# Performance work log

Hardware: AMD Instinct MI355X
Metric: run time of the kernel (lower is better)

## Reference

```python
import jax, jax.numpy as jnp
import numpy as np

N_C, N_S, D = 16384, 16384, 2688  # 128x128 hypercolumn grid, VGG16 concat channels
EPS = 1e-8


def setup_inputs() -> dict:
    key = jax.random.key(0)
    k1, k2 = jax.random.split(key)
    feats_c = jax.random.normal(k1, (N_C, D), dtype=jnp.float32)
    feats_s = jax.random.normal(k2, (N_S, D), dtype=jnp.float32)
    return {"feats_c": feats_c, "feats_s": feats_s}


def reference(feats_c, feats_s):
    # NNST replace_features: for each content hypercolumn vector, find the
    # style feature vector with max cosine similarity and take it as target.
    cn = feats_c * jax.lax.rsqrt(jnp.sum(feats_c * feats_c, axis=1, keepdims=True) + EPS)
    sn = feats_s * jax.lax.rsqrt(jnp.sum(feats_s * feats_s, axis=1, keepdims=True) + EPS)
    sim = jnp.einsum("cd,sd->cs", cn, sn)  # [N_C, N_S] cosine similarity
    idx = jnp.argmax(sim, axis=1)           # nearest style feature per content pixel
    target_feats = jnp.take(feats_s, idx, axis=0)  # gather un-normalized style feats
    return target_feats
```

## Files before the change

kernel.cpp:

```cpp
#include <hip/hip_runtime.h>
#include <stdint.h>

typedef unsigned short ushort_t;
typedef unsigned int u32;
typedef unsigned long long u64;

#define NC_ 16384
#define NS_ 16384
#define DIM 2688
#define D4 (DIM / 4)
#define KSTEPS (DIM / 32)

typedef __attribute__((ext_vector_type(8))) short short8;
typedef __attribute__((ext_vector_type(4))) float f32x4;


__device__ inline ushort_t f2bf(float x) {
  u32 u = __float_as_uint(x);
  u32 r = u + 0x7FFFu + ((u >> 16) & 1u);
  return (ushort_t)(r >> 16);
}
__device__ inline float bf2f(ushort_t b) { return __uint_as_float(((u32)b) << 16); }

__device__ inline u32 fkey(float f) {
  u32 u = __float_as_uint(f);
  return (u & 0x80000000u) ? ~u : (u | 0x80000000u);
}

__device__ inline void async16(const void* g, void* l) {
  __builtin_amdgcn_global_load_lds(
      (const __attribute__((address_space(1))) u32*)g,
      (__attribute__((address_space(3))) u32*)l, 16, 0, 0);
}

__device__ inline int swz(int r, int q) {
  return ((r >> 1) << 6) + (((((r & 1) << 2) | q) ^ ((r >> 1) & 7)) << 3);
}


__global__ __launch_bounds__(256) void content_split_kernel(
    const float* __restrict__ fc, ushort_t* __restrict__ c_hi, ushort_t* __restrict__ c_lo) {
  size_t i = (size_t)blockIdx.x * 256 + threadIdx.x;
  if (i >= (size_t)NC_ * DIM / 4) return;
  float4 v = ((const float4*)fc)[i];
  ushort4 h, l;
  h.x = f2bf(v.x); l.x = f2bf(v.x - bf2f(h.x));
  h.y = f2bf(v.y); l.y = f2bf(v.y - bf2f(h.y));
  h.z = f2bf(v.z); l.z = f2bf(v.z - bf2f(h.z));
  h.w = f2bf(v.w); l.w = f2bf(v.w - bf2f(h.w));
  ((ushort4*)c_hi)[i] = h;
  ((ushort4*)c_lo)[i] = l;
}


__global__ __launch_bounds__(256) void style_split_kernel(
    const float* __restrict__ fs, ushort_t* __restrict__ s_hi, ushort_t* __restrict__ s_lo) {
  const int s = blockIdx.x, t = threadIdx.x;
  const float4* row = (const float4*)(fs + (size_t)s * DIM);
  float ss = 0.f;
  for (int i = t; i < D4; i += 256) {
    float4 v = row[i];
    ss += v.x * v.x + v.y * v.y + v.z * v.z + v.w * v.w;
  }
#pragma unroll
  for (int off = 32; off >= 1; off >>= 1) ss += __shfl_xor(ss, off, 64);
  __shared__ float wsum[4];
  if ((t & 63) == 0) wsum[t >> 6] = ss;
  __syncthreads();
  float scale = rsqrtf(wsum[0] + wsum[1] + wsum[2] + wsum[3] + 1e-8f);
  ushort4* h4 = (ushort4*)(s_hi + (size_t)s * DIM);
  ushort4* l4 = (ushort4*)(s_lo + (size_t)s * DIM);
  for (int i = t; i < D4; i += 256) {
    float4 v = row[i];
    float x = v.x * scale, y = v.y * scale, z = v.z * scale, w = v.w * scale;
    ushort4 h, l;
    h.x = f2bf(x); l.x = f2bf(x - bf2f(h.x));
    h.y = f2bf(y); l.y = f2bf(y - bf2f(h.y));
    h.z = f2bf(z); l.z = f2bf(z - bf2f(h.z));
    h.w = f2bf(w); l.w = f2bf(w - bf2f(h.w));
    h4[i] = h;
    l4[i] = l;
  }
}


__global__ __launch_bounds__(256, 2) void sim_argmax_kernel(
    const ushort_t* __restrict__ c_hi, const ushort_t* __restrict__ c_lo,
    const ushort_t* __restrict__ s_hi, const ushort_t* __restrict__ s_lo,
    u64* __restrict__ partial) {
  __shared__ __align__(16) ushort_t lds[24576];

  ushort_t* la_hi = lds;
  ushort_t* la_lo = lds + 4096;
  ushort_t* lb_hi = lds + 8192;
  ushort_t* lb_lo = lds + 16384;
  u64 (*red)[2] = (u64(*)[2])lds;

  const int t = threadIdx.x;
  const int bid = blockIdx.x;
  const int grp = bid >> 8;
  const int wi = bid & 255;
  const int cb = (grp & 7) * 16 + (wi & 15);
  const int sb = (grp >> 3) * 16 + (wi >> 4);

  const ushort_t* gah = c_hi + (size_t)cb * 128 * DIM;
  const ushort_t* gal = c_lo + (size_t)cb * 128 * DIM;
  const ushort_t* gbh = s_hi + (size_t)sb * 256 * DIM;
  const ushort_t* gbl = s_lo + (size_t)sb * 256 * DIM;

  const int lane = t & 63;
  const int wave = t >> 6;
  const int wy = wave >> 1, wx = wave & 1;
  const int lm = lane & 15, q = lane >> 4;

  f32x4 acc[4][8];
#pragma unroll
  for (int i = 0; i < 4; i++)
#pragma unroll
    for (int j = 0; j < 8; j++) acc[i][j] = (f32x4){0.f, 0.f, 0.f, 0.f};

  const int tw = t & 192;

  for (int ks = 0; ks < KSTEPS; ++ks) {
    const int kel = ks * 32;
#pragma unroll
    for (int j = 0; j < 2; ++j) {
      int e = j * 256 + t;
      int rp = e >> 3;
      int cc = (e & 7) ^ (rp & 7);
      int row = (rp << 1) | (cc >> 2);
      size_t goff = (size_t)row * DIM + kel + (cc & 3) * 8;
      int loff = (j * 256 + tw) * 8;
      async16(gah + goff, la_hi + loff);
      async16(gal + goff, la_lo + loff);
    }
#pragma unroll
    for (int j = 0; j < 4; ++j) {
      int e = j * 256 + t;
      int rp = e >> 3;
      int cc = (e & 7) ^ (rp & 7);
      int row = (rp << 1) | (cc >> 2);
      size_t goff = (size_t)row * DIM + kel + (cc & 3) * 8;
      int loff = (j * 256 + tw) * 8;
      async16(gbh + goff, lb_hi + loff);
      async16(gbl + goff, lb_lo + loff);
    }
    __syncthreads();

    short8 ah[4], al[4];
#pragma unroll
    for (int mi = 0; mi < 4; ++mi) {
      int r = swz(wy * 64 + mi * 16 + lm, q);
      ah[mi] = *(const short8*)(la_hi + r);
      al[mi] = *(const short8*)(la_lo + r);
    }
#pragma unroll
    for (int h = 0; h < 2; ++h) {
      short8 bh[4], bl[4];
#pragma unroll
      for (int nj = 0; nj < 4; ++nj) {
        int r = swz(wx * 128 + (h * 4 + nj) * 16 + lm, q);
        bh[nj] = *(const short8*)(lb_hi + r);
        bl[nj] = *(const short8*)(lb_lo + r);
      }
#pragma unroll
      for (int mi = 0; mi < 4; ++mi)
#pragma unroll
        for (int nj = 0; nj < 4; ++nj) {
          int ni = h * 4 + nj;
          acc[mi][ni] = __builtin_amdgcn_mfma_f32_16x16x32_bf16(ah[mi], bh[nj], acc[mi][ni], 0, 0, 0);
          acc[mi][ni] = __builtin_amdgcn_mfma_f32_16x16x32_bf16(ah[mi], bl[nj], acc[mi][ni], 0, 0, 0);
          acc[mi][ni] = __builtin_amdgcn_mfma_f32_16x16x32_bf16(al[mi], bh[nj], acc[mi][ni], 0, 0, 0);
        }
    }
    __syncthreads();
  }

#pragma unroll
  for (int mi = 0; mi < 4; ++mi) {
#pragma unroll
    for (int r = 0; r < 4; ++r) {
      float bv = acc[mi][0][r];
      int bn = 0;
#pragma unroll
      for (int ni = 1; ni < 8; ++ni) {
        float v = acc[mi][ni][r];
        if (v > bv) { bv = v; bn = ni; }
      }
      u32 colg = (u32)(sb * 256 + wx * 128 + bn * 16 + lm);
      u64 key = ((u64)fkey(bv) << 32) | (u64)(0xFFFFFFFFu - colg);
#pragma unroll
      for (int off = 8; off >= 1; off >>= 1) {
        u64 o = __shfl_xor((unsigned long long)key, off, 64);
        if (o > key) key = o;
      }
      if (lm == 0) red[wy * 64 + mi * 16 + q * 4 + r][wx] = key;
    }
  }
  __syncthreads();
  if (t < 128) {
    u64 k0 = red[t][0], k1 = red[t][1];
    u64 b = k0 > k1 ? k0 : k1;
    partial[((size_t)(cb * 128 + t)) * 64 + sb] = b;
  }
}


__global__ __launch_bounds__(256) void argmax_gather_kernel(
    const u64* __restrict__ partial, const float* __restrict__ fs, float* __restrict__ out) {
  const int m = blockIdx.x, t = threadIdx.x;
  __shared__ u64 sbest;
  if (t < 64) {
    u64 key = partial[(size_t)m * 64 + t];
#pragma unroll
    for (int off = 32; off >= 1; off >>= 1) {
      u64 o = __shfl_xor((unsigned long long)key, off, 64);
      if (o > key) key = o;
    }
    if (t == 0) sbest = key;
  }
  __syncthreads();
  u64 best = sbest;
  u32 col = 0xFFFFFFFFu - (u32)best;
  const float4* src = (const float4*)(fs + (size_t)col * DIM);
  float4* dst = (float4*)(out + (size_t)m * DIM);
  for (int i = t; i < D4; i += 256) dst[i] = src[i];
}


extern "C" void kernel_launch(void* const* d_in, const int* in_sizes, int n_in,
                              void* d_out, int out_size, void* d_ws, size_t ws_size,
                              hipStream_t stream) {
  const float* fc = (const float*)d_in[0];
  const float* fs = (const float*)d_in[1];
  float* out = (float*)d_out;

  ushort_t* c_hi = (ushort_t*)d_ws;
  ushort_t* c_lo = c_hi + (size_t)NC_ * DIM;
  ushort_t* s_hi = c_lo + (size_t)NC_ * DIM;
  ushort_t* s_lo = s_hi + (size_t)NS_ * DIM;
  u64* partial = (u64*)(s_lo + (size_t)NS_ * DIM);

  content_split_kernel<<<(NC_ * DIM / 4 + 255) / 256, 256, 0, stream>>>(fc, c_hi, c_lo);
  style_split_kernel<<<NS_, 256, 0, stream>>>(fs, s_hi, s_lo);
  sim_argmax_kernel<<<8192, 256, 0, stream>>>(c_hi, c_lo, s_hi, s_lo, partial);
  argmax_gather_kernel<<<NC_, 256, 0, stream>>>(partial, fs, out);
}
```

Before: 3.799 ms.

## Enlarge similarity tile to 256x256 with double-buffered async LDS prefetch

The similarity/argmax kernel now uses 512-thread blocks computing 256x256 content-by-style tiles, instead of 256-thread blocks on 128x256 tiles. This raises data reuse per loaded K-slice. The LDS is split into two buffers so the global-to-LDS async loads for step k+1 are issued before computing step k. A vmcnt wait plus barriers replace the per-step syncthreads. The larger LDS footprint (about 136KB) likely allows only one block per CU, so occupancy drops, and the cross-wave reduction grows to four columns.

```diff
diff --git a/kernel.cpp b/kernel.cpp
--- a/kernel.cpp
+++ b/kernel.cpp
@@ -84,124 +84,122 @@
 }
 
 
-__global__ __launch_bounds__(256, 2) void sim_argmax_kernel(
+__global__ __launch_bounds__(512, 2) void sim_argmax_kernel(
     const ushort_t* __restrict__ c_hi, const ushort_t* __restrict__ c_lo,
     const ushort_t* __restrict__ s_hi, const ushort_t* __restrict__ s_lo,
     u64* __restrict__ partial) {
-  __shared__ __align__(16) ushort_t lds[24576];
-
-  ushort_t* la_hi = lds;
-  ushort_t* la_lo = lds + 4096;
-  ushort_t* lb_hi = lds + 8192;
-  ushort_t* lb_lo = lds + 16384;
-  u64 (*red)[2] = (u64(*)[2])lds;
+  __shared__ __align__(16) ushort_t lds[65536];
+  __shared__ u64 red[256][4];
 
   const int t = threadIdx.x;
   const int bid = blockIdx.x;
-  const int grp = bid >> 8;
-  const int wi = bid & 255;
-  const int cb = (grp & 7) * 16 + (wi & 15);
-  const int sb = (grp >> 3) * 16 + (wi >> 4);
-
-  const ushort_t* gah = c_hi + (size_t)cb * 128 * DIM;
-  const ushort_t* gal = c_lo + (size_t)cb * 128 * DIM;
+  const int grp = bid >> 6;
+  const int wi = bid & 63;
+  const int cb = (grp & 7) * 8 + (wi & 7);
+  const int sb = (grp >> 3) * 8 + (wi >> 3);
+
+  const ushort_t* gah = c_hi + (size_t)cb * 256 * DIM;
+  const ushort_t* gal = c_lo + (size_t)cb * 256 * DIM;
   const ushort_t* gbh = s_hi + (size_t)sb * 256 * DIM;
   const ushort_t* gbl = s_lo + (size_t)sb * 256 * DIM;
 
   const int lane = t & 63;
   const int wave = t >> 6;
-  const int wy = wave >> 1, wx = wave & 1;
+  const int wy = wave >> 2, wx = wave & 3;
   const int lm = lane & 15, q = lane >> 4;
-
-  f32x4 acc[4][8];
-#pragma unroll
-  for (int i = 0; i < 4; i++)
-#pragma unroll
-    for (int j = 0; j < 8; j++) acc[i][j] = (f32x4){0.f, 0.f, 0.f, 0.f};
-
-  const int tw = t & 192;
-
-  for (int ks = 0; ks < KSTEPS; ++ks) {
+  const int wb = t & 448;
+
+  f32x4 acc[8][4];
+#pragma unroll
+  for (int i = 0; i < 8; i++)
+#pragma unroll
+    for (int j = 0; j < 4; j++) acc[i][j] = (f32x4){0.f, 0.f, 0.f, 0.f};
+
+  auto stage = [&](int ks, int b) {
     const int kel = ks * 32;
+    ushort_t* base = lds + b * 32768;
 #pragma unroll
     for (int j = 0; j < 2; ++j) {
-      int e = j * 256 + t;
+      int e = j * 512 + t;
       int rp = e >> 3;
       int cc = (e & 7) ^ (rp & 7);
       int row = (rp << 1) | (cc >> 2);
       size_t goff = (size_t)row * DIM + kel + (cc & 3) * 8;
-      int loff = (j * 256 + tw) * 8;
-      async16(gah + goff, la_hi + loff);
-      async16(gal + goff, la_lo + loff);
-    }
-#pragma unroll
-    for (int j = 0; j < 4; ++j) {
-      int e = j * 256 + t;
-      int rp = e >> 3;
-      int cc = (e & 7) ^ (rp & 7);
-      int row = (rp << 1) | (cc >> 2);
-      size_t goff = (size_t)row * DIM + kel + (cc & 3) * 8;
-      int loff = (j * 256 + tw) * 8;
-      async16(gbh + goff, lb_hi + loff);
-      async16(gbl + goff, lb_lo + loff);
-    }
-    __syncthreads();
-
-    short8 ah[4], al[4];
-#pragma unroll
-    for (int mi = 0; mi < 4; ++mi) {
-      int r = swz(wy * 64 + mi * 16 + lm, q);
-      ah[mi] = *(const short8*)(la_hi + r);
-      al[mi] = *(const short8*)(la_lo + r);
-    }
-#pragma unroll
-    for (int h = 0; h < 2; ++h) {
-      short8 bh[4], bl[4];
-#pragma unroll
-      for (int nj = 0; nj < 4; ++nj) {
-        int r = swz(wx * 128 + (h * 4 + nj) * 16 + lm, q);
-        bh[nj] = *(const short8*)(lb_hi + r);
-        bl[nj] = *(const short8*)(lb_lo + r);
+      int loff = (j * 512 + wb) * 8;
+      async16(gah + goff, base + loff);
+      async16(gal + goff, base + 8192 + loff);
+      async16(gbh + goff, base + 16384 + loff);
+      async16(gbl + goff, base + 24576 + loff);
+    }
+  };
+
+  auto compute = [&](int b) {
+    ushort_t* base = lds + b * 32768;
+    const ushort_t* lah = base;
+    const ushort_t* lal = base + 8192;
+    const ushort_t* lbh = base + 16384;
+    const ushort_t* lbl = base + 24576;
+    short8 ah[8], al[8];
+#pragma unroll
+    for (int mi = 0; mi < 8; ++mi) {
+      int r = swz(wy * 128 + mi * 16 + lm, q);
+      ah[mi] = *(const short8*)(lah + r);
+      al[mi] = *(const short8*)(lal + r);
+    }
+#pragma unroll
+    for (int nj = 0; nj < 4; ++nj) {
+      int r = swz(wx * 64 + nj * 16 + lm, q);
+      short8 bh = *(const short8*)(lbh + r);
+      short8 bl = *(const short8*)(lbl + r);
+#pragma unroll
+      for (int mi = 0; mi < 8; ++mi) {
+        acc[mi][nj] = __builtin_amdgcn_mfma_f32_16x16x32_bf16(ah[mi], bh, acc[mi][nj], 0, 0, 0);
+        acc[mi][nj] = __builtin_amdgcn_mfma_f32_16x16x32_bf16(ah[mi], bl, acc[mi][nj], 0, 0, 0);
+        acc[mi][nj] = __builtin_amdgcn_mfma_f32_16x16x32_bf16(al[mi], bh, acc[mi][nj], 0, 0, 0);
       }
-#pragma unroll
-      for (int mi = 0; mi < 4; ++mi)
-#pragma unroll
-        for (int nj = 0; nj < 4; ++nj) {
-          int ni = h * 4 + nj;
-          acc[mi][ni] = __builtin_amdgcn_mfma_f32_16x16x32_bf16(ah[mi], bh[nj], acc[mi][ni], 0, 0, 0);
-          acc[mi][ni] = __builtin_amdgcn_mfma_f32_16x16x32_bf16(ah[mi], bl[nj], acc[mi][ni], 0, 0, 0);
-          acc[mi][ni] = __builtin_amdgcn_mfma_f32_16x16x32_bf16(al[mi], bh[nj], acc[mi][ni], 0, 0, 0);
-        }
-    }
-    __syncthreads();
-  }
-
-#pragma unroll
-  for (int mi = 0; mi < 4; ++mi) {
+    }
+  };
+
+  stage(0, 0);
+  for (int ks = 0; ks < KSTEPS - 1; ++ks) {
+    stage(ks + 1, (ks + 1) & 1);
+    asm volatile("s_waitcnt vmcnt(8)" ::: "memory");
+    __builtin_amdgcn_s_barrier();
+    compute(ks & 1);
+    __builtin_amdgcn_s_barrier();
+  }
+  asm volatile("s_waitcnt vmcnt(0)" ::: "memory");
+  __builtin_amdgcn_s_barrier();
+  compute((KSTEPS - 1) & 1);
+
+#pragma unroll
+  for (int mi = 0; mi < 8; ++mi) {
 #pragma unroll
     for (int r = 0; r < 4; ++r) {
       float bv = acc[mi][0][r];
       int bn = 0;
 #pragma unroll
-      for (int ni = 1; ni < 8; ++ni) {
-        float v = acc[mi][ni][r];
-        if (v > bv) { bv = v; bn = ni; }
+      for (int nj = 1; nj < 4; ++nj) {
+        float v = acc[mi][nj][r];
+        if (v > bv) { bv = v; bn = nj; }
       }
-      u32 colg = (u32)(sb * 256 + wx * 128 + bn * 16 + lm);
+      u32 colg = (u32)(sb * 256 + wx * 64 + bn * 16 + lm);
       u64 key = ((u64)fkey(bv) << 32) | (u64)(0xFFFFFFFFu - colg);
 #pragma unroll
       for (int off = 8; off >= 1; off >>= 1) {
         u64 o = __shfl_xor((unsigned long long)key, off, 64);
         if (o > key) key = o;
       }
-      if (lm == 0) red[wy * 64 + mi * 16 + q * 4 + r][wx] = key;
+      if (lm == 0) red[wy * 128 + mi * 16 + q * 4 + r][wx] = key;
     }
   }
   __syncthreads();
-  if (t < 128) {
-    u64 k0 = red[t][0], k1 = red[t][1];
-    u64 b = k0 > k1 ? k0 : k1;
-    partial[((size_t)(cb * 128 + t)) * 64 + sb] = b;
+  if (t < 256) {
+    u64 k0 = red[t][0], k1 = red[t][1], k2 = red[t][2], k3 = red[t][3];
+    u64 a = k0 > k1 ? k0 : k1;
+    u64 c = k2 > k3 ? k2 : k3;
+    u64 b = a > c ? a : c;
+    partial[((size_t)(cb * 256 + t)) * 64 + sb] = b;
   }
 }
 
@@ -243,6 +241,6 @@
 
   content_split_kernel<<<(NC_ * DIM / 4 + 255) / 256, 256, 0, stream>>>(fc, c_hi, c_lo);
   style_split_kernel<<<NS_, 256, 0, stream>>>(fs, s_hi, s_lo);
-  sim_argmax_kernel<<<8192, 256, 0, stream>>>(c_hi, c_lo, s_hi, s_lo, partial);
+  sim_argmax_kernel<<<4096, 512, 0, stream>>>(c_hi, c_lo, s_hi, s_lo, partial);
   argmax_gather_kernel<<<NC_, 256, 0, stream>>>(partial, fs, out);
 }
```

After: 3.765 ms. About the same (-0.9%).
